# Kernel optimization log

Measured on AMD Instinct MI355X. Metric: run time of the kernel, lower is better.

## Reference

```python
import jax, jax.numpy as jnp
import numpy as np
import math

NUM_HEADS = 8
EMB = 256

def setup_inputs() -> dict:
    key = jax.random.key(0)
    ks = jax.random.split(key, 9)
    B_, N, C = 1024, 64, EMB  # 16 images * 64 windows, 8x8 window, C=256
    nW = 64
    q = jax.random.normal(ks[0], (B_, N, C), dtype=jnp.float32)
    k = jax.random.normal(ks[1], (B_, N, C), dtype=jnp.float32)
    v = jax.random.normal(ks[2], (B_, N, C), dtype=jnp.float32)
    mask = jax.random.normal(ks[3], (nW, N, N), dtype=jnp.float32)
    # MLP params (Linear: y = x @ W^T + b; we store W already transposed for x @ W)
    hid = 4 * C
    s1 = 1.0 / math.sqrt(C)
    s2 = 1.0 / math.sqrt(hid)
    w1 = jax.random.uniform(ks[4], (C, hid), minval=-s1, maxval=s1, dtype=jnp.float32)
    b1 = jax.random.uniform(ks[5], (hid,), minval=-s1, maxval=s1, dtype=jnp.float32)
    w2 = jax.random.uniform(ks[6], (hid, C), minval=-s2, maxval=s2, dtype=jnp.float32)
    b2 = jax.random.uniform(ks[7], (C,), minval=-s2, maxval=s2, dtype=jnp.float32)
    return {"q": q, "k": k, "v": v, "mask": mask, "H": 64, "W": 64,
            "w1": w1, "b1": b1, "w2": w2, "b2": b2}

def reference(q, k, v, mask, H, W, w1, b1, w2, b2):
    B_, N, C = q.shape
    h = NUM_HEADS
    d = C // h
    # separate heads: (B_, h, N, d)
    qh = q.reshape(B_, N, h, d).transpose(0, 2, 1, 3)
    kh = k.reshape(B_, N, h, d).transpose(0, 2, 1, 3)
    vh = v.reshape(B_, N, h, d).transpose(0, 2, 1, 3)
    attn = jnp.einsum('bhnd,bhmd->bhnm', qh, kh)  # raw scores
    nW = mask.shape[0]
    # additive window mask BEFORE scaling (faithful to original order)
    attn = attn.reshape(B_ // nW, nW, h, N, N) + mask[None, :, None, :, :]
    attn = attn.reshape(B_, h, N, N) / math.sqrt(d)
    attn = jax.nn.softmax(attn, axis=-1)
    out = jnp.einsum('bhnm,bhmd->bhnd', attn, vh)
    out = out.transpose(0, 2, 1, 3).reshape(B_, N, C)  # recombine heads
    # linear Mlp (dropout is identity at p=0.0); torch nn.GELU is exact erf
    hmid = jax.nn.gelu(out @ w1 + b1, approximate=False)
    out = out + (hmid @ w2 + b2)
    return out
```

## Files before the change

### kernel.cpp

```cpp
#include <hip/hip_runtime.h>
#include <hip/hip_bf16.h>
#include <cstdint>
#include <cstddef>

typedef __attribute__((ext_vector_type(8))) short bf16x8;
typedef __attribute__((ext_vector_type(4))) float f32x4;
typedef __attribute__((ext_vector_type(16))) float f32x16;

static __device__ __forceinline__ unsigned short f2bf(float f) {
    __hip_bfloat16 h = __float2bfloat16(f);
    return *reinterpret_cast<unsigned short*>(&h);
}

static __device__ __forceinline__ f32x4 mfma_bf16(bf16x8 a, bf16x8 b, f32x4 c) {
    return __builtin_amdgcn_mfma_f32_16x16x32_bf16(a, b, c, 0, 0, 0);
}
static __device__ __forceinline__ f32x16 mfma32(bf16x8 a, bf16x8 b, f32x16 c) {
    return __builtin_amdgcn_mfma_f32_32x32x16_bf16(a, b, c, 0, 0, 0);
}

static __device__ __forceinline__ bf16x8 pack8(float4 a, float4 b) {
    bf16x8 f;
    f[0]=(short)f2bf(a.x); f[1]=(short)f2bf(a.y); f[2]=(short)f2bf(a.z); f[3]=(short)f2bf(a.w);
    f[4]=(short)f2bf(b.x); f[5]=(short)f2bf(b.y); f[6]=(short)f2bf(b.z); f[7]=(short)f2bf(b.w);
    return f;
}

static __device__ __forceinline__ float gelu_erf(float v) {
    float s = v * 0.70710678118654752f;
    float a = fabsf(s);
    float t = __builtin_amdgcn_rcpf(1.0f + 0.3275911f * a);
    float poly = ((((1.061405429f * t - 1.453152027f) * t + 1.421413741f) * t
                   - 0.284496736f) * t + 0.254829592f) * t;
    float e = 1.0f - poly * __expf(-a * a);
    float erfv = copysignf(e, s);
    return 0.5f * v * (1.0f + erfv);
}

static __device__ __forceinline__ void load_lds16(const unsigned short* g, unsigned short* l) {
    __builtin_amdgcn_global_load_lds(
        (const __attribute__((address_space(1))) unsigned int*)g,
        (__attribute__((address_space(3))) unsigned int*)l, 16, 0, 0);
}

__global__ __launch_bounds__(256) void attn_kernel(
    const float* __restrict__ q, const float* __restrict__ k,
    const float* __restrict__ v, const float* __restrict__ mask,
    float* __restrict__ xout)
{
    __shared__ unsigned short Qs[64][40];
    __shared__ unsigned short Ks[64][40];
    __shared__ unsigned short Vt[32][72];
    __shared__ unsigned short Ps[64][72];

    const int tid  = threadIdx.x;
    const int b    = blockIdx.x >> 3;
    const int h    = blockIdx.x & 7;
    const int lane = tid & 63;
    const int l15  = lane & 15;
    const int g    = lane >> 4;
    const int w    = tid >> 6;

    {
        int row = tid >> 2;
        int seg = tid & 3;
        size_t base = ((size_t)(b * 64 + row)) * 256 + h * 32 + seg * 8;

        float4 a0 = *(const float4*)(q + base);
        float4 a1 = *(const float4*)(q + base + 4);
        unsigned short* p = &Qs[row][seg * 8];
        p[0]=f2bf(a0.x); p[1]=f2bf(a0.y); p[2]=f2bf(a0.z); p[3]=f2bf(a0.w);
        p[4]=f2bf(a1.x); p[5]=f2bf(a1.y); p[6]=f2bf(a1.z); p[7]=f2bf(a1.w);

        a0 = *(const float4*)(k + base);
        a1 = *(const float4*)(k + base + 4);
        p = &Ks[row][seg * 8];
        p[0]=f2bf(a0.x); p[1]=f2bf(a0.y); p[2]=f2bf(a0.z); p[3]=f2bf(a0.w);
        p[4]=f2bf(a1.x); p[5]=f2bf(a1.y); p[6]=f2bf(a1.z); p[7]=f2bf(a1.w);

        a0 = *(const float4*)(v + base);
        a1 = *(const float4*)(v + base + 4);
        int c = seg * 8;
        Vt[c + 0][row] = f2bf(a0.x);
        Vt[c + 1][row] = f2bf(a0.y);
        Vt[c + 2][row] = f2bf(a0.z);
        Vt[c + 3][row] = f2bf(a0.w);
        Vt[c + 4][row] = f2bf(a1.x);
        Vt[c + 5][row] = f2bf(a1.y);
        Vt[c + 6][row] = f2bf(a1.z);
        Vt[c + 7][row] = f2bf(a1.w);
    }
    __syncthreads();

    f32x4 s[4];
    {
        bf16x8 aQ = *(const bf16x8*)&Qs[w * 16 + l15][g * 8];
        #pragma unroll
        for (int ct = 0; ct < 4; ++ct) {
            bf16x8 bK = *(const bf16x8*)&Ks[ct * 16 + l15][g * 8];
            f32x4 z = {0.f, 0.f, 0.f, 0.f};
            s[ct] = mfma_bf16(aQ, bK, z);
        }
    }

    const float* mbase = mask + (size_t)(b & 63) * 4096;
    const float INV = 0.17677669529663688f;
    float rsum[4];
    #pragma unroll
    for (int r = 0; r < 4; ++r) {
        int row = w * 16 + g * 4 + r;
        float pr[4];
        #pragma unroll
        for (int ct = 0; ct < 4; ++ct)
            pr[ct] = (s[ct][r] + mbase[row * 64 + ct * 16 + l15]) * INV;
        float m = fmaxf(fmaxf(pr[0], pr[1]), fmaxf(pr[2], pr[3]));
        #pragma unroll
        for (int off = 1; off < 16; off <<= 1)
            m = fmaxf(m, __shfl_xor(m, off));
        float sum = 0.f;
        #pragma unroll
        for (int ct = 0; ct < 4; ++ct) { pr[ct] = __expf(pr[ct] - m); sum += pr[ct]; }
        #pragma unroll
        for (int off = 1; off < 16; off <<= 1)
            sum += __shfl_xor(sum, off);
        rsum[r] = sum;
        #pragma unroll
        for (int ct = 0; ct < 4; ++ct)
            Ps[row][ct * 16 + l15] = f2bf(pr[ct]);
    }

    f32x4 o[2] = {};
    #pragma unroll
    for (int ks = 0; ks < 2; ++ks) {
        bf16x8 pa = *(const bf16x8*)&Ps[w * 16 + l15][ks * 32 + g * 8];
        #pragma unroll
        for (int n = 0; n < 2; ++n) {
            bf16x8 vb = *(const bf16x8*)&Vt[n * 16 + l15][ks * 32 + g * 8];
            o[n] = mfma_bf16(pa, vb, o[n]);
        }
    }

    #pragma unroll
    for (int n = 0; n < 2; ++n) {
        #pragma unroll
        for (int r = 0; r < 4; ++r) {
            int row = w * 16 + g * 4 + r;
            xout[((size_t)(b * 64 + row)) * 256 + h * 32 + n * 16 + l15] =
                o[n][r] / rsum[r];
        }
    }
}

static __device__ __forceinline__ int sigma32(int a) {
    return ((a >> 4) & 1) * 16 + ((a >> 2) & 1) * 8 + ((a >> 3) & 1) * 4 + (a & 3);
}

__global__ __launch_bounds__(256) void prep_w1(const float* __restrict__ src,
                                               unsigned short* __restrict__ dst)
{
    const int c = blockIdx.x;
    const int t = threadIdx.x;
    #pragma unroll
    for (int i = 0; i < 4; ++i) {
        int idx = i * 256 + t;
        int ks  = idx >> 6;
        int l   = idx & 63;
        int l31 = l & 31, hi = l >> 5;
        int n   = c * 32 + sigma32(l31);
        unsigned short tmp[8];
        #pragma unroll
        for (int e = 0; e < 8; ++e)
            tmp[e] = f2bf(src[(size_t)(ks * 16 + hi * 8 + e) * 1024 + n]);
        *(bf16x8*)(dst + (size_t)c * 8192 + ks * 512 + l * 8) = *(const bf16x8*)tmp;
    }
}

__global__ __launch_bounds__(256) void prep_w2(const float* __restrict__ src,
                                               unsigned short* __restrict__ dst)
{
    const int c = blockIdx.x;
    const int t = threadIdx.x;
    #pragma unroll
    for (int i = 0; i < 4; ++i) {
        int idx  = i * 256 + t;
        int span = idx >> 6;
        int l    = idx & 63;
        int n    = span >> 1;
        int j    = span & 1;
        int l31  = l & 31, hi = l >> 5;
        unsigned short tmp[8];
        #pragma unroll
        for (int e = 0; e < 8; ++e)
            tmp[e] = f2bf(src[(size_t)(c * 32 + j * 16 + hi * 8 + e) * 256 + n * 32 + l31]);
        *(bf16x8*)(dst + (size_t)c * 8192 + span * 512 + l * 8) = *(const bf16x8*)tmp;
    }
}

__global__ __launch_bounds__(256, 2) void mlp_fused(
    const float* __restrict__ xin, float* __restrict__ xio,
    const unsigned short* __restrict__ wt1, const float* __restrict__ b1,
    const unsigned short* __restrict__ wt2, const float* __restrict__ b2)
{
    __shared__ unsigned short w1c[2][8192];
    __shared__ unsigned short w2c[2][8192];
    __shared__ float b1s[1024];

    const int tid  = threadIdx.x;
    const int lane = tid & 63;
    const int l31  = lane & 31;
    const int hi   = lane >> 5;
    const int wid  = tid >> 6;
    const int fb   = lane * 8;

    const size_t rowbase = (size_t)blockIdx.x * 128 + wid * 32;

    auto stage = [&](const unsigned short* gbase, unsigned short* lbase) {
        #pragma unroll
        for (int i = 0; i < 4; ++i) {
            load_lds16(gbase + (i * 256 + tid) * 8,
                       lbase + (i * 256 + wid * 64) * 8);
        }
    };

    stage(wt1, &w1c[0][0]);
    stage(wt2, &w2c[0][0]);

    b1s[tid]       = b1[tid];
    b1s[tid + 256] = b1[tid + 256];
    b1s[tid + 512] = b1[tid + 512];
    b1s[tid + 768] = b1[tid + 768];

    bf16x8 xf[16];
    {
        const float* xr = xin + (rowbase + l31) * 256;
        #pragma unroll
        for (int ks = 0; ks < 16; ++ks) {
            float4 a0 = *(const float4*)(xr + ks * 16 + hi * 8);
            float4 a1 = *(const float4*)(xr + ks * 16 + hi * 8 + 4);
            xf[ks] = pack8(a0, a1);
        }
    }

    f32x16 oacc[8] = {};

    for (int c = 0; c < 32; ++c) {
        const int cur = c & 1;
        __syncthreads();

        if (c < 31) {
            stage(wt1 + (size_t)(c + 1) * 8192, &w1c[cur ^ 1][0]);
            stage(wt2 + (size_t)(c + 1) * 8192, &w2c[cur ^ 1][0]);
        }

        f32x16 hacc = {};
        #pragma unroll
        for (int ks = 0; ks < 16; ++ks) {
            bf16x8 wf = *(const bf16x8*)&w1c[cur][ks * 512 + fb];
            hacc = mfma32(wf, xf[ks], hacc);
        }

        const float* bp = &b1s[c * 32 + hi * 8];
        float4 ba0 = *(const float4*)(bp);
        float4 ba1 = *(const float4*)(bp + 4);
        float4 bb0 = *(const float4*)(bp + 16);
        float4 bb1 = *(const float4*)(bp + 20);
        bf16x8 aH0, aH1;
        aH0[0] = (short)f2bf(gelu_erf(hacc[0]  + ba0.x));
        aH0[1] = (short)f2bf(gelu_erf(hacc[1]  + ba0.y));
        aH0[2] = (short)f2bf(gelu_erf(hacc[2]  + ba0.z));
        aH0[3] = (short)f2bf(gelu_erf(hacc[3]  + ba0.w));
        aH0[4] = (short)f2bf(gelu_erf(hacc[4]  + ba1.x));
        aH0[5] = (short)f2bf(gelu_erf(hacc[5]  + ba1.y));
        aH0[6] = (short)f2bf(gelu_erf(hacc[6]  + ba1.z));
        aH0[7] = (short)f2bf(gelu_erf(hacc[7]  + ba1.w));
        aH1[0] = (short)f2bf(gelu_erf(hacc[8]  + bb0.x));
        aH1[1] = (short)f2bf(gelu_erf(hacc[9]  + bb0.y));
        aH1[2] = (short)f2bf(gelu_erf(hacc[10] + bb0.z));
        aH1[3] = (short)f2bf(gelu_erf(hacc[11] + bb0.w));
        aH1[4] = (short)f2bf(gelu_erf(hacc[12] + bb1.x));
        aH1[5] = (short)f2bf(gelu_erf(hacc[13] + bb1.y));
        aH1[6] = (short)f2bf(gelu_erf(hacc[14] + bb1.z));
        aH1[7] = (short)f2bf(gelu_erf(hacc[15] + bb1.w));

        #pragma unroll
        for (int n = 0; n < 8; ++n) {
            bf16x8 bF0 = *(const bf16x8*)&w2c[cur][(n * 2 + 0) * 512 + fb];
            bf16x8 bF1 = *(const bf16x8*)&w2c[cur][(n * 2 + 1) * 512 + fb];
            oacc[n] = mfma32(aH0, bF0, oacc[n]);
            oacc[n] = mfma32(aH1, bF1, oacc[n]);
        }
    }

    #pragma unroll
    for (int n = 0; n < 8; ++n) {
        int col = n * 32 + l31;
        float bias = b2[col];
        #pragma unroll
        for (int r = 0; r < 16; ++r) {
            int row_local = (r & 3) + 8 * (r >> 2) + 4 * hi;
            size_t idx = (rowbase + row_local) * 256 + col;
            xio[idx] = oacc[n][r] + bias + xio[idx];
        }
    }
}

extern "C" void kernel_launch(void* const* d_in, const int* in_sizes, int n_in,
                              void* d_out, int out_size, void* d_ws, size_t ws_size,
                              hipStream_t stream)
{
    const float* q    = (const float*)d_in[0];
    const float* k    = (const float*)d_in[1];
    const float* v    = (const float*)d_in[2];
    const float* mask = (const float*)d_in[3];
    const float* w1   = (const float*)d_in[6];
    const float* b1   = (const float*)d_in[7];
    const float* w2   = (const float*)d_in[8];
    const float* b2   = (const float*)d_in[9];

    float* xio = (float*)d_out;

    unsigned short* wt1 = (unsigned short*)d_ws;
    unsigned short* wt2 = wt1 + (size_t)1024 * 256;

    prep_w1<<<32, 256, 0, stream>>>(w1, wt1);
    prep_w2<<<32, 256, 0, stream>>>(w2, wt2);

    attn_kernel<<<8192, 256, 0, stream>>>(q, k, v, mask, xio);

    mlp_fused<<<512, 256, 0, stream>>>(xio, xio, wt1, b1, wt2, b2);
}
```

Baseline: 163.7 us.

## Double MLP block size and chunk width, fold bias into accumulator, cheaper erf

The fused MLP kernel now runs 512 threads per block covering 256 rows, and each pipeline step stages two 32-wide hidden chunks of both weight matrices, so there are half as many barriers and the staged weights are shared by twice as many rows. The first-layer bias is loaded into the accumulator before the MFMA chain instead of being added afterwards. The erf inside GELU switches from the 5-term Abramowitz-Stegun polynomial to the 3-term version, which cuts ALU work but raises the approximation error to about 2.5e-5. Shared memory per block roughly doubles to about 132 KB, which may allow only one block per CU despite the launch bound of 2.

```diff
diff --git a/kernel.cpp b/kernel.cpp
--- a/kernel.cpp
+++ b/kernel.cpp
@@ -29,9 +29,8 @@
 static __device__ __forceinline__ float gelu_erf(float v) {
     float s = v * 0.70710678118654752f;
     float a = fabsf(s);
-    float t = __builtin_amdgcn_rcpf(1.0f + 0.3275911f * a);
-    float poly = ((((1.061405429f * t - 1.453152027f) * t + 1.421413741f) * t
-                   - 0.284496736f) * t + 0.254829592f) * t;
+    float t = __builtin_amdgcn_rcpf(1.0f + 0.47047f * a);
+    float poly = ((0.7478556f * t - 0.0958798f) * t + 0.3480242f) * t;
     float e = 1.0f - poly * __expf(-a * a);
     float erfv = copysignf(e, s);
     return 0.5f * v * (1.0f + erfv);
@@ -196,13 +195,13 @@
     }
 }
 
-__global__ __launch_bounds__(256, 2) void mlp_fused(
+__global__ __launch_bounds__(512, 2) void mlp_fused(
     const float* __restrict__ xin, float* __restrict__ xio,
     const unsigned short* __restrict__ wt1, const float* __restrict__ b1,
     const unsigned short* __restrict__ wt2, const float* __restrict__ b2)
 {
-    __shared__ unsigned short w1c[2][8192];
-    __shared__ unsigned short w2c[2][8192];
+    __shared__ unsigned short w1c[2][16384];
+    __shared__ unsigned short w2c[2][16384];
     __shared__ float b1s[1024];
 
     const int tid  = threadIdx.x;
@@ -212,13 +211,13 @@
     const int wid  = tid >> 6;
     const int fb   = lane * 8;
 
-    const size_t rowbase = (size_t)blockIdx.x * 128 + wid * 32;
+    const size_t rowbase = (size_t)blockIdx.x * 256 + wid * 32;
 
     auto stage = [&](const unsigned short* gbase, unsigned short* lbase) {
         #pragma unroll
         for (int i = 0; i < 4; ++i) {
-            load_lds16(gbase + (i * 256 + tid) * 8,
-                       lbase + (i * 256 + wid * 64) * 8);
+            load_lds16(gbase + (i * 512 + tid) * 8,
+                       lbase + (i * 512 + wid * 64) * 8);
         }
     };
 
@@ -226,9 +225,7 @@
     stage(wt2, &w2c[0][0]);
 
     b1s[tid]       = b1[tid];
-    b1s[tid + 256] = b1[tid + 256];
     b1s[tid + 512] = b1[tid + 512];
-    b1s[tid + 768] = b1[tid + 768];
 
     bf16x8 xf[16];
     {
@@ -243,44 +240,54 @@
 
     f32x16 oacc[8] = {};
 
-    for (int c = 0; c < 32; ++c) {
-        const int cur = c & 1;
+    auto bias_init = [&](int c) -> f32x16 {
+        const float* bp = &b1s[c * 32 + hi * 8];
+        float4 b0 = *(const float4*)(bp);
+        float4 b1v = *(const float4*)(bp + 4);
+        float4 b2v = *(const float4*)(bp + 16);
+        float4 b3 = *(const float4*)(bp + 20);
+        f32x16 h;
+        h[0]=b0.x;  h[1]=b0.y;  h[2]=b0.z;  h[3]=b0.w;
+        h[4]=b1v.x; h[5]=b1v.y; h[6]=b1v.z; h[7]=b1v.w;
+        h[8]=b2v.x; h[9]=b2v.y; h[10]=b2v.z; h[11]=b2v.w;
+        h[12]=b3.x; h[13]=b3.y; h[14]=b3.z; h[15]=b3.w;
+        return h;
+    };
+
+    for (int i = 0; i < 16; ++i) {
+        const int cur = i & 1;
         __syncthreads();
 
-        if (c < 31) {
-            stage(wt1 + (size_t)(c + 1) * 8192, &w1c[cur ^ 1][0]);
-            stage(wt2 + (size_t)(c + 1) * 8192, &w2c[cur ^ 1][0]);
-        }
-
-        f32x16 hacc = {};
+        if (i < 15) {
+            stage(wt1 + (size_t)(i + 1) * 16384, &w1c[cur ^ 1][0]);
+            stage(wt2 + (size_t)(i + 1) * 16384, &w2c[cur ^ 1][0]);
+        }
+
+        f32x16 haccA = bias_init(2 * i);
         #pragma unroll
         for (int ks = 0; ks < 16; ++ks) {
             bf16x8 wf = *(const bf16x8*)&w1c[cur][ks * 512 + fb];
-            hacc = mfma32(wf, xf[ks], hacc);
-        }
-
-        const float* bp = &b1s[c * 32 + hi * 8];
-        float4 ba0 = *(const float4*)(bp);
-        float4 ba1 = *(const float4*)(bp + 4);
-        float4 bb0 = *(const float4*)(bp + 16);
-        float4 bb1 = *(const float4*)(bp + 20);
+            haccA = mfma32(wf, xf[ks], haccA);
+        }
         bf16x8 aH0, aH1;
-        aH0[0] = (short)f2bf(gelu_erf(hacc[0]  + ba0.x));
-        aH0[1] = (short)f2bf(gelu_erf(hacc[1]  + ba0.y));
-        aH0[2] = (short)f2bf(gelu_erf(hacc[2]  + ba0.z));
-        aH0[3] = (short)f2bf(gelu_erf(hacc[3]  + ba0.w));
-        aH0[4] = (short)f2bf(gelu_erf(hacc[4]  + ba1.x));
-        aH0[5] = (short)f2bf(gelu_erf(hacc[5]  + ba1.y));
-        aH0[6] = (short)f2bf(gelu_erf(hacc[6]  + ba1.z));
-        aH0[7] = (short)f2bf(gelu_erf(hacc[7]  + ba1.w));
-        aH1[0] = (short)f2bf(gelu_erf(hacc[8]  + bb0.x));
-        aH1[1] = (short)f2bf(gelu_erf(hacc[9]  + bb0.y));
-        aH1[2] = (short)f2bf(gelu_erf(hacc[10] + bb0.z));
-        aH1[3] = (short)f2bf(gelu_erf(hacc[11] + bb0.w));
-        aH1[4] = (short)f2bf(gelu_erf(hacc[12] + bb1.x));
-        aH1[5] = (short)f2bf(gelu_erf(hacc[13] + bb1.y));
-        aH1[6] = (short)f2bf(gelu_erf(hacc[14] + bb1.z));
-        aH1[7] = (short)f2bf(gelu_erf(hacc[15] + bb1.w));
+        #pragma unroll
+        for (int e = 0; e < 8; ++e) {
+            aH0[e] = (short)f2bf(gelu_erf(haccA[e]));
+            aH1[e] = (short)f2bf(gelu_erf(haccA[e + 8]));
+        }
+
+        f32x16 haccB = bias_init(2 * i + 1);
+        #pragma unroll
+        for (int ks = 0; ks < 16; ++ks) {
+            bf16x8 wf = *(const bf16x8*)&w1c[cur][(16 + ks) * 512 + fb];
+            haccB = mfma32(wf, xf[ks], haccB);
+        }
+        bf16x8 cH0, cH1;
+        #pragma unroll
+        for (int e = 0; e < 8; ++e) {
+            cH0[e] = (short)f2bf(gelu_erf(haccB[e]));
+            cH1[e] = (short)f2bf(gelu_erf(haccB[e + 8]));
+        }
 
         #pragma unroll
         for (int n = 0; n < 8; ++n) {
@@ -288,6 +295,13 @@
             bf16x8 bF1 = *(const bf16x8*)&w2c[cur][(n * 2 + 1) * 512 + fb];
             oacc[n] = mfma32(aH0, bF0, oacc[n]);
             oacc[n] = mfma32(aH1, bF1, oacc[n]);
+        }
+        #pragma unroll
+        for (int n = 0; n < 8; ++n) {
+            bf16x8 bF0 = *(const bf16x8*)&w2c[cur][(16 + n * 2 + 0) * 512 + fb];
+            bf16x8 bF1 = *(const bf16x8*)&w2c[cur][(16 + n * 2 + 1) * 512 + fb];
+            oacc[n] = mfma32(cH0, bF0, oacc[n]);
+            oacc[n] = mfma32(cH1, bF1, oacc[n]);
         }
     }
 
@@ -327,5 +341,5 @@
 
     attn_kernel<<<8192, 256, 0, stream>>>(q, k, v, mask, xio);
 
-    mlp_fused<<<512, 256, 0, stream>>>(xio, xio, wt1, b1, wt2, b2);
-}
+    mlp_fused<<<256, 512, 0, stream>>>(xio, xio, wt1, b1, wt2, b2);
+}
```

Result: no change. 163.6 us (-0.1%).

## Store attention output as bf16 intermediate and cheapen GELU, fold bias into accumulator

Applied to the files above, without the earlier changes.

The attention kernel now writes its output as bf16 into a workspace buffer, and the MLP kernel reads it directly as MFMA operands and for the residual. This halves the intermediate traffic and removes the fp32-to-bf16 conversion in the MLP. The erf approximation drops from a 5-term to a 3-term polynomial, the b1 bias is preloaded into the accumulator, and s_setprio is placed around the MFMA blocks. The risks are lower accuracy in both the residual path (now bf16) and the GELU, plus a dependence on workspace size.

```diff
diff --git a/kernel.cpp b/kernel.cpp
--- a/kernel.cpp
+++ b/kernel.cpp
@@ -10,6 +10,10 @@
 static __device__ __forceinline__ unsigned short f2bf(float f) {
     __hip_bfloat16 h = __float2bfloat16(f);
     return *reinterpret_cast<unsigned short*>(&h);
+}
+static __device__ __forceinline__ float bf2f(unsigned short u) {
+    union { unsigned int i; float f; } x; x.i = ((unsigned int)u) << 16;
+    return x.f;
 }
 
 static __device__ __forceinline__ f32x4 mfma_bf16(bf16x8 a, bf16x8 b, f32x4 c) {
@@ -29,9 +33,8 @@
 static __device__ __forceinline__ float gelu_erf(float v) {
     float s = v * 0.70710678118654752f;
     float a = fabsf(s);
-    float t = __builtin_amdgcn_rcpf(1.0f + 0.3275911f * a);
-    float poly = ((((1.061405429f * t - 1.453152027f) * t + 1.421413741f) * t
-                   - 0.284496736f) * t + 0.254829592f) * t;
+    float t = __builtin_amdgcn_rcpf(1.0f + 0.47047f * a);
+    float poly = ((0.7478556f * t - 0.0958798f) * t + 0.3480242f) * t;
     float e = 1.0f - poly * __expf(-a * a);
     float erfv = copysignf(e, s);
     return 0.5f * v * (1.0f + erfv);
@@ -43,10 +46,11 @@
         (__attribute__((address_space(3))) unsigned int*)l, 16, 0, 0);
 }
 
+template <bool BF16X>
 __global__ __launch_bounds__(256) void attn_kernel(
     const float* __restrict__ q, const float* __restrict__ k,
     const float* __restrict__ v, const float* __restrict__ mask,
-    float* __restrict__ xout)
+    float* __restrict__ xo_f, unsigned short* __restrict__ xo_b)
 {
     __shared__ unsigned short Qs[64][40];
     __shared__ unsigned short Ks[64][40];
@@ -145,8 +149,10 @@
         #pragma unroll
         for (int r = 0; r < 4; ++r) {
             int row = w * 16 + g * 4 + r;
-            xout[((size_t)(b * 64 + row)) * 256 + h * 32 + n * 16 + l15] =
-                o[n][r] / rsum[r];
+            size_t idx = ((size_t)(b * 64 + row)) * 256 + h * 32 + n * 16 + l15;
+            float val = o[n][r] / rsum[r];
+            if (BF16X) xo_b[idx] = f2bf(val);
+            else       xo_f[idx] = val;
         }
     }
 }
@@ -196,8 +202,10 @@
     }
 }
 
+template <bool BF16X>
 __global__ __launch_bounds__(256, 2) void mlp_fused(
-    const float* __restrict__ xin, float* __restrict__ xio,
+    const float* __restrict__ xin_f, const unsigned short* __restrict__ xin_b,
+    float* __restrict__ out,
     const unsigned short* __restrict__ wt1, const float* __restrict__ b1,
     const unsigned short* __restrict__ wt2, const float* __restrict__ b2)
 {
@@ -231,8 +239,13 @@
     b1s[tid + 768] = b1[tid + 768];
 
     bf16x8 xf[16];
-    {
-        const float* xr = xin + (rowbase + l31) * 256;
+    if (BF16X) {
+        const unsigned short* xr = xin_b + (rowbase + l31) * 256;
+        #pragma unroll
+        for (int ks = 0; ks < 16; ++ks)
+            xf[ks] = *(const bf16x8*)(xr + ks * 16 + hi * 8);
+    } else {
+        const float* xr = xin_f + (rowbase + l31) * 256;
         #pragma unroll
         for (int ks = 0; ks < 16; ++ks) {
             float4 a0 = *(const float4*)(xr + ks * 16 + hi * 8);
@@ -252,36 +265,35 @@
             stage(wt2 + (size_t)(c + 1) * 8192, &w2c[cur ^ 1][0]);
         }
 
-        f32x16 hacc = {};
+        f32x16 hacc;
+        {
+            const float* bp = &b1s[c * 32 + hi * 8];
+            float4 b0 = *(const float4*)(bp);
+            float4 b1v = *(const float4*)(bp + 4);
+            float4 b2v = *(const float4*)(bp + 16);
+            float4 b3 = *(const float4*)(bp + 20);
+            hacc[0]=b0.x;  hacc[1]=b0.y;  hacc[2]=b0.z;  hacc[3]=b0.w;
+            hacc[4]=b1v.x; hacc[5]=b1v.y; hacc[6]=b1v.z; hacc[7]=b1v.w;
+            hacc[8]=b2v.x; hacc[9]=b2v.y; hacc[10]=b2v.z; hacc[11]=b2v.w;
+            hacc[12]=b3.x; hacc[13]=b3.y; hacc[14]=b3.z; hacc[15]=b3.w;
+        }
+
+        __builtin_amdgcn_s_setprio(1);
         #pragma unroll
         for (int ks = 0; ks < 16; ++ks) {
             bf16x8 wf = *(const bf16x8*)&w1c[cur][ks * 512 + fb];
             hacc = mfma32(wf, xf[ks], hacc);
         }
-
-        const float* bp = &b1s[c * 32 + hi * 8];
-        float4 ba0 = *(const float4*)(bp);
-        float4 ba1 = *(const float4*)(bp + 4);
-        float4 bb0 = *(const float4*)(bp + 16);
-        float4 bb1 = *(const float4*)(bp + 20);
+        __builtin_amdgcn_s_setprio(0);
+
         bf16x8 aH0, aH1;
-        aH0[0] = (short)f2bf(gelu_erf(hacc[0]  + ba0.x));
-        aH0[1] = (short)f2bf(gelu_erf(hacc[1]  + ba0.y));
-        aH0[2] = (short)f2bf(gelu_erf(hacc[2]  + ba0.z));
-        aH0[3] = (short)f2bf(gelu_erf(hacc[3]  + ba0.w));
-        aH0[4] = (short)f2bf(gelu_erf(hacc[4]  + ba1.x));
-        aH0[5] = (short)f2bf(gelu_erf(hacc[5]  + ba1.y));
-        aH0[6] = (short)f2bf(gelu_erf(hacc[6]  + ba1.z));
-        aH0[7] = (short)f2bf(gelu_erf(hacc[7]  + ba1.w));
-        aH1[0] = (short)f2bf(gelu_erf(hacc[8]  + bb0.x));
-        aH1[1] = (short)f2bf(gelu_erf(hacc[9]  + bb0.y));
-        aH1[2] = (short)f2bf(gelu_erf(hacc[10] + bb0.z));
-        aH1[3] = (short)f2bf(gelu_erf(hacc[11] + bb0.w));
-        aH1[4] = (short)f2bf(gelu_erf(hacc[12] + bb1.x));
-        aH1[5] = (short)f2bf(gelu_erf(hacc[13] + bb1.y));
-        aH1[6] = (short)f2bf(gelu_erf(hacc[14] + bb1.z));
-        aH1[7] = (short)f2bf(gelu_erf(hacc[15] + bb1.w));
-
+        #pragma unroll
+        for (int e = 0; e < 8; ++e) {
+            aH0[e] = (short)f2bf(gelu_erf(hacc[e]));
+            aH1[e] = (short)f2bf(gelu_erf(hacc[e + 8]));
+        }
+
+        __builtin_amdgcn_s_setprio(1);
         #pragma unroll
         for (int n = 0; n < 8; ++n) {
             bf16x8 bF0 = *(const bf16x8*)&w2c[cur][(n * 2 + 0) * 512 + fb];
@@ -289,6 +301,7 @@
             oacc[n] = mfma32(aH0, bF0, oacc[n]);
             oacc[n] = mfma32(aH1, bF1, oacc[n]);
         }
+        __builtin_amdgcn_s_setprio(0);
     }
 
     #pragma unroll
@@ -299,7 +312,8 @@
         for (int r = 0; r < 16; ++r) {
             int row_local = (r & 3) + 8 * (r >> 2) + 4 * hi;
             size_t idx = (rowbase + row_local) * 256 + col;
-            xio[idx] = oacc[n][r] + bias + xio[idx];
+            float resid = BF16X ? bf2f(xin_b[idx]) : xin_f[idx];
+            out[idx] = oacc[n][r] + bias + resid;
         }
     }
 }
@@ -317,15 +331,22 @@
     const float* w2   = (const float*)d_in[8];
     const float* b2   = (const float*)d_in[9];
 
-    float* xio = (float*)d_out;
+    float* out = (float*)d_out;
 
     unsigned short* wt1 = (unsigned short*)d_ws;
     unsigned short* wt2 = wt1 + (size_t)1024 * 256;
+    unsigned short* xbf = wt2 + (size_t)1024 * 256;
+
+    const size_t need = (size_t)2 * 1024 * 256 * 2 + (size_t)65536 * 256 * 2;
 
     prep_w1<<<32, 256, 0, stream>>>(w1, wt1);
     prep_w2<<<32, 256, 0, stream>>>(w2, wt2);
 
-    attn_kernel<<<8192, 256, 0, stream>>>(q, k, v, mask, xio);
-
-    mlp_fused<<<512, 256, 0, stream>>>(xio, xio, wt1, b1, wt2, b2);
-}
+    if (ws_size >= need) {
+        attn_kernel<true><<<8192, 256, 0, stream>>>(q, k, v, mask, nullptr, xbf);
+        mlp_fused<true><<<512, 256, 0, stream>>>(nullptr, xbf, out, wt1, b1, wt2, b2);
+    } else {
+        attn_kernel<false><<<8192, 256, 0, stream>>>(q, k, v, mask, out, nullptr);
+        mlp_fused<false><<<512, 256, 0, stream>>>(out, nullptr, out, wt1, b1, wt2, b2);
+    }
+}
```

New measurement: 158.8 us. -3.0%, faster.
